# Optimization experiments

Measured on AMD Instinct MI355X. Metric: run time of the kernel, lower is better.

## Reference

```python
import jax, jax.numpy as jnp
import numpy as np
import math

D = 1024
B, S = 8, 2048


def setup_inputs() -> dict:
    key = jax.random.key(0)
    ks = jax.random.split(key, 8)
    q = jax.random.normal(ks[0], (B, S, D), dtype=jnp.float32)
    k = jax.random.normal(ks[1], (B, S, D), dtype=jnp.float32)
    v1 = jax.random.normal(ks[2], (B, S, D), dtype=jnp.float32)
    mask = jax.random.normal(ks[3], (1, S, S), dtype=jnp.float32)
    # Linear params: torch Linear stores W as [out, in]; init ~ U(-1/sqrt(in), 1/sqrt(in))
    lim = 1.0 / math.sqrt(D)
    W1 = jax.random.uniform(ks[4], (D, D), jnp.float32, -lim, lim)
    b1 = jax.random.uniform(ks[5], (D,), jnp.float32, -lim, lim)
    W2 = jax.random.uniform(ks[6], (D, D), jnp.float32, -lim, lim)
    b2 = jax.random.uniform(ks[7], (D,), jnp.float32, -lim, lim)
    return {"q": q, "k": k, "v1": v1, "mask": mask,
            "W1": W1, "b1": b1, "W2": W2, "b2": b2}


def _proj(x, W1, b1, W2, b2):
    # linear2(linear1(x)); torch Linear: x @ W.T + b
    h = jnp.einsum('bsd,od->bso', x, W1) + b1
    return jnp.einsum('bsd,od->bso', h, W2) + b2


def reference(q, k, v1, mask, W1, b1, W2, b2):
    qp = _proj(q, W1, b1, W2, b2)          # [B,S,D]
    kp = _proj(k, W1, b1, W2, b2)          # [B,S,D]
    scale = 1.0 / math.sqrt(qp.shape[-1])
    qk = jnp.einsum('bqd,bkd->bqk', qp, kp) * scale  # [B,S,S]
    qk = qk + mask                          # broadcast [1,S,S]
    attn = jax.nn.softmax(qk, axis=-1)
    return jnp.einsum('bqk,bkd->bqd', attn, v1)  # [B,S,D]
```

## Files before the change

### kernel.cpp

```cpp
#include <hip/hip_runtime.h>
#include <hip/hip_bf16.h>

typedef __hip_bfloat16 bf16;
typedef short short8 __attribute__((ext_vector_type(8)));
typedef float f32x4 __attribute__((ext_vector_type(4)));

constexpr int Bn = 8, Sn = 2048, Dn = 1024;
constexpr int BM = 256, BN = 256, BK = 64;

__global__ void cast_f32_bf16_k(const float* __restrict__ x, bf16* __restrict__ y, int n) {
  int i = (blockIdx.x * blockDim.x + threadIdx.x) * 4;
  if (i >= n) return;
  float4 f = *reinterpret_cast<const float4*>(x + i);
  bf16 tmp[4] = {__float2bfloat16(f.x), __float2bfloat16(f.y),
                 __float2bfloat16(f.z), __float2bfloat16(f.w)};
  *reinterpret_cast<short4*>(y + i) = *reinterpret_cast<const short4*>(tmp);
}

__global__ void transpose_cast_v_k(const float* __restrict__ v, bf16* __restrict__ vt) {
  __shared__ float tile[32][33];
  const int s0 = blockIdx.x * 32, d0 = blockIdx.y * 32, b = blockIdx.z;
  const float* src = v + (size_t)b * Sn * Dn;
  bf16* dst = vt + (size_t)b * Dn * Sn;
  const int tx = threadIdx.x & 31, ty = threadIdx.x >> 5;
  #pragma unroll
  for (int i = 0; i < 4; ++i) {
    int s = ty + i * 8;
    tile[s][tx] = src[(size_t)(s0 + s) * Dn + d0 + tx];
  }
  __syncthreads();
  #pragma unroll
  for (int i = 0; i < 4; ++i) {
    int d = ty + i * 8;
    dst[(size_t)(d0 + d) * Sn + s0 + tx] = __float2bfloat16(tile[tx][d]);
  }
}

#define BARRIER() asm volatile("s_barrier" ::: "memory")
#define WAIT_VM8() asm volatile("s_waitcnt vmcnt(8)" ::: "memory")
#define WAIT_VM0() asm volatile("s_waitcnt vmcnt(0)" ::: "memory")

#define QUAD(ms, ns) do {                                                     \
    __builtin_amdgcn_s_setprio(1);                                            \
    _Pragma("unroll")                                                         \
    for (int kk = 0; kk < 2; ++kk) {                                          \
      _Pragma("unroll")                                                       \
      for (int mi4 = 0; mi4 < 4; ++mi4) {                                     \
        _Pragma("unroll")                                                     \
        for (int n2 = 0; n2 < 2; ++n2)                                        \
          asm volatile("v_mfma_f32_16x16x32_bf16 %0, %1, %2, %0"              \
                       : "+v"(acc[(ms)*4+mi4][(ns)*2+n2])                     \
                       : "v"(aF[mi4][kk]), "v"(bF[(ns)*2+n2][kk]));           \
      }                                                                       \
    }                                                                         \
    __builtin_amdgcn_s_setprio(0);                                            \
  } while (0)

#define RD_A(buf, ms) do {                                                    \
    _Pragma("unroll")                                                         \
    for (int mi4 = 0; mi4 < 4; ++mi4) {                                       \
      aF[mi4][0] = rdA(buf, ms, mi4, 0);                                      \
      aF[mi4][1] = rdA(buf, ms, mi4, 1);                                      \
    }                                                                         \
  } while (0)

#define RD_B(buf, ns) do {                                                    \
    bF[(ns)*2  ][0] = rdB(buf, ns, 0, 0);                                     \
    bF[(ns)*2  ][1] = rdB(buf, ns, 0, 1);                                     \
    bF[(ns)*2+1][0] = rdB(buf, ns, 1, 0);                                     \
    bF[(ns)*2+1][1] = rdB(buf, ns, 1, 1);                                     \
  } while (0)

#define TILE_BODY(cc, DS, Tn2, WAITCODE) do {                                 \
    RD_A(cc, 0); RD_B(cc, 0);                                                 \
    BARRIER(); QUAD(0, 0); BARRIER();                                         \
    RD_B(cc, 1);                                                              \
    BARRIER(); QUAD(0, 1); BARRIER();                                         \
    RD_A(cc, 1);                                                              \
    if (DS) stage(32768 + (cc)*16384, Bbase, 0, (Tn2));                       \
    BARRIER(); QUAD(1, 0); BARRIER();                                         \
    if (DS) { stage(32768 + (cc)*16384, Bbase, 1, (Tn2));                     \
              stage((cc)*16384,          Abase, 0, (Tn2));                    \
              stage((cc)*16384,          Abase, 1, (Tn2)); }                  \
    BARRIER(); QUAD(1, 1);                                                    \
    WAITCODE;                                                                 \
    BARRIER();                                                                \
  } while (0)

template<int EPI>
__global__ __launch_bounds__(512, 2)
void gemm256_k(const bf16* __restrict__ A, const bf16* __restrict__ BT,
               void* __restrict__ Cv, const float* __restrict__ aux,
               int N, int K, long long sAz, long long sBz, long long sCz,
               float scale, int gx, int gy)
{
  __shared__ __align__(128) bf16 sh[4 * 16384];

  const int nwg = (int)gridDim.x;
  const int flat = (int)blockIdx.x;
  const int swz = (flat & 7) * (nwg >> 3) + (flat >> 3);
  const int tn = swz % gx;
  const int rem = swz / gx;
  const int tm = rem % gy;
  const int z  = rem / gy;

  const int t = threadIdx.x, w = t >> 6, lane = t & 63;
  const int wm = w >> 2, wn = w & 3;
  const int fr = lane & 15, kg = lane >> 4;
  const int m0 = tm * BM, n0 = tn * BN;
  const bf16* Abase = A + (size_t)z * sAz + (size_t)m0 * K;
  const bf16* Bbase = BT + (size_t)z * sBz + (size_t)n0 * K;

  f32x4 acc[8][4];
  const f32x4 fz = {0.f, 0.f, 0.f, 0.f};
  #pragma unroll
  for (int i = 0; i < 8; ++i)
    #pragma unroll
    for (int j = 0; j < 4; ++j) acc[i][j] = fz;
  short8 aF[4][2], bF[4][2];

  auto stage = [&](int dstElemBase, const bf16* gbase, int half, int kt) {
    const bf16* g0 = gbase + (size_t)(half * 128) * K + (size_t)kt * BK;
    bf16* db = (bf16*)sh + dstElemBase + half * 8192;
    #pragma unroll
    for (int i = 0; i < 2; ++i) {
      const int s0 = i * 512 + w * 64;
      const int slot = s0 + lane;
      const int row = slot >> 3;
      const int cb = (slot & 7) ^ (row & 7);
      const bf16* src = g0 + (size_t)row * K + cb * 8;
      __builtin_amdgcn_global_load_lds((__attribute__((address_space(1))) void*)src,
          (__attribute__((address_space(3))) void*)(db + s0 * 8), 16, 0, 0);
    }
  };
  auto rdA = [&](int buf, int ms, int mi4, int kk) -> short8 {
    const int row = wm * 128 + ms * 64 + mi4 * 16 + fr;
    int loc = row * 128 + kk * 64 + kg * 16;
    loc ^= (row & 7) << 4;
    return *reinterpret_cast<const short8*>((const char*)sh + buf * 32768 + loc);
  };
  auto rdB = [&](int buf, int ns, int j, int kk) -> short8 {
    const int row = wn * 64 + ns * 32 + j * 16 + fr;
    int loc = row * 128 + kk * 64 + kg * 16;
    loc ^= (row & 7) << 4;
    return *reinterpret_cast<const short8*>((const char*)sh + 65536 + buf * 32768 + loc);
  };

  const int NT = K / BK;
  stage(32768, Bbase, 0, 0); stage(32768, Bbase, 1, 0);
  stage(0,     Abase, 0, 0); stage(0,     Abase, 1, 0);
  stage(49152, Bbase, 0, 1); stage(49152, Bbase, 1, 1);
  stage(16384, Abase, 0, 1); stage(16384, Abase, 1, 1);
  WAIT_VM8();
  BARRIER();

  int T = 0;
  for (; T < NT - 2; T += 2) {
    TILE_BODY(0, (T     < NT - 2), T + 2, WAIT_VM8());
    TILE_BODY(1, (T + 1 < NT - 2), T + 3, WAIT_VM8());
  }
  TILE_BODY(0, 0, 0, WAIT_VM0());
  TILE_BODY(1, 0, 0, (void)0);

  const int or0 = kg * 4;
  if constexpr (EPI == 0) {
    bf16* C = (bf16*)Cv + (size_t)z * sCz;
    #pragma unroll
    for (int mi = 0; mi < 8; ++mi)
      #pragma unroll
      for (int r = 0; r < 4; ++r) {
        const int row = m0 + wm * 128 + mi * 16 + or0 + r;
        #pragma unroll
        for (int ni = 0; ni < 4; ++ni) {
          const int col = n0 + wn * 64 + ni * 16 + fr;
          C[(size_t)row * N + col] = __float2bfloat16(acc[mi][ni][r] + aux[col]);
        }
      }
  } else if constexpr (EPI == 1) {
    bf16* C = (bf16*)Cv + (size_t)z * sCz;
    #pragma unroll
    for (int mi = 0; mi < 8; ++mi)
      #pragma unroll
      for (int r = 0; r < 4; ++r) {
        const int row = m0 + wm * 128 + mi * 16 + or0 + r;
        #pragma unroll
        for (int ni = 0; ni < 4; ++ni) {
          const int col = n0 + wn * 64 + ni * 16 + fr;
          float v = acc[mi][ni][r] * scale + aux[(size_t)row * N + col];
          C[(size_t)row * N + col] = __float2bfloat16(v);
        }
      }
  } else {
    float* C = (float*)Cv + (size_t)z * sCz;
    #pragma unroll
    for (int mi = 0; mi < 8; ++mi)
      #pragma unroll
      for (int r = 0; r < 4; ++r) {
        const int row = m0 + wm * 128 + mi * 16 + or0 + r;
        #pragma unroll
        for (int ni = 0; ni < 4; ++ni) {
          const int col = n0 + wn * 64 + ni * 16 + fr;
          C[(size_t)row * N + col] = acc[mi][ni][r];
        }
      }
  }
}

__global__ __launch_bounds__(256)
void softmax_rows_k(bf16* __restrict__ sc) {
  const size_t row = blockIdx.x;
  bf16* p = sc + row * (size_t)Sn;
  const int t = threadIdx.x;
  unsigned short raw[8];
  *reinterpret_cast<int4*>(raw) = *reinterpret_cast<const int4*>(p + t * 8);
  float x[8];
  float m = -1e30f;
  #pragma unroll
  for (int j = 0; j < 8; ++j) {
    x[j] = __uint_as_float(((unsigned)raw[j]) << 16);
    m = fmaxf(m, x[j]);
  }
  #pragma unroll
  for (int off = 32; off >= 1; off >>= 1) m = fmaxf(m, __shfl_xor(m, off));
  __shared__ float sred[4], ssum[4];
  const int w = t >> 6;
  if ((t & 63) == 0) sred[w] = m;
  __syncthreads();
  m = fmaxf(fmaxf(sred[0], sred[1]), fmaxf(sred[2], sred[3]));
  float e[8], s = 0.f;
  #pragma unroll
  for (int j = 0; j < 8; ++j) { e[j] = __expf(x[j] - m); s += e[j]; }
  #pragma unroll
  for (int off = 32; off >= 1; off >>= 1) s += __shfl_xor(s, off);
  if ((t & 63) == 0) ssum[w] = s;
  __syncthreads();
  s = (ssum[0] + ssum[1]) + (ssum[2] + ssum[3]);
  const float inv = 1.f / s;
  unsigned short o[8];
  #pragma unroll
  for (int j = 0; j < 8; ++j) {
    bf16 hv = __float2bfloat16(e[j] * inv);
    o[j] = *reinterpret_cast<unsigned short*>(&hv);
  }
  *reinterpret_cast<int4*>(p + t * 8) = *reinterpret_cast<const int4*>(o);
}

extern "C" void kernel_launch(void* const* d_in, const int* in_sizes, int n_in,
                              void* d_out, int out_size, void* d_ws, size_t ws_size,
                              hipStream_t stream) {
  const float* q    = (const float*)d_in[0];
  const float* k    = (const float*)d_in[1];
  const float* v1   = (const float*)d_in[2];
  const float* mask = (const float*)d_in[3];
  const float* W1   = (const float*)d_in[4];
  const float* b1   = (const float*)d_in[5];
  const float* W2   = (const float*)d_in[6];
  const float* b2   = (const float*)d_in[7];
  float* out = (float*)d_out;

  const size_t nQKD = (size_t)Bn * Sn * Dn;
  char* ws = (char*)d_ws;
  bf16* qkb = (bf16*)ws;
  bf16* qb  = qkb;
  bf16* kb  = qkb + nQKD;
  bf16* vtb = qkb + 2 * nQKD;
  bf16* hb  = vtb + nQKD;
  bf16* w1b = hb + 2 * nQKD;
  bf16* w2b = w1b + (size_t)Dn * Dn;
  bf16* scb = w2b + (size_t)Dn * Dn;

  dim3 blk(256);
  const int nQK = (int)nQKD;
  cast_f32_bf16_k<<<dim3(nQK / 4 / 256), blk, 0, stream>>>(q, qb, nQK);
  cast_f32_bf16_k<<<dim3(nQK / 4 / 256), blk, 0, stream>>>(k, kb, nQK);
  cast_f32_bf16_k<<<dim3(Dn * Dn / 4 / 256), blk, 0, stream>>>(W1, w1b, Dn * Dn);
  cast_f32_bf16_k<<<dim3(Dn * Dn / 4 / 256), blk, 0, stream>>>(W2, w2b, Dn * Dn);
  transpose_cast_v_k<<<dim3(Sn / 32, Dn / 32, Bn), blk, 0, stream>>>(v1, vtb);

  const int M2 = 2 * Bn * Sn;
  dim3 gblk(512);
  gemm256_k<0><<<dim3(4 * (M2 / BM)), gblk, 0, stream>>>(
      qkb, w1b, hb, b1, Dn, Dn, 0, 0, 0, 1.f, 4, M2 / BM);
  gemm256_k<0><<<dim3(4 * (M2 / BM)), gblk, 0, stream>>>(
      hb, w2b, qkb, b2, Dn, Dn, 0, 0, 0, 1.f, 4, M2 / BM);
  gemm256_k<1><<<dim3(8 * 8 * Bn), gblk, 0, stream>>>(
      qb, kb, scb, mask, Sn, Dn,
      (long long)Sn * Dn, (long long)Sn * Dn, (long long)Sn * Sn, 0.03125f, 8, 8);
  softmax_rows_k<<<dim3(Bn * Sn), blk, 0, stream>>>(scb);
  gemm256_k<2><<<dim3(4 * 8 * Bn), gblk, 0, stream>>>(
      scb, vtb, out, nullptr, Dn, Sn,
      (long long)Sn * Sn, (long long)Dn * Sn, (long long)Sn * Dn, 1.f, 4, 8);
}
```

Measured before the change: 398.3 us.

## Interleave global-to-LDS prefetch stages across each quadrant of the GEMM main loop

Restructures the 256x256 GEMM main loop so that the global_load_lds prefetches for A and B are spread one per MFMA quadrant instead of grouped, with staggered tiles (A for T+1, B for T+2) and a vmcnt(4) wait instead of vmcnt(8). It also replaces inline-asm MFMA with the compiler builtin and adds explicit lgkmcnt(0) waits before each quadrant. The aim is to smooth memory issue and let the compiler schedule MFMAs, at the cost of more barriers and waits that could stall the waves.

```diff
diff --git a/kernel.cpp b/kernel.cpp
--- a/kernel.cpp
+++ b/kernel.cpp
@@ -2,7 +2,7 @@
 #include <hip/hip_bf16.h>
 
 typedef __hip_bfloat16 bf16;
-typedef short short8 __attribute__((ext_vector_type(8)));
+typedef __bf16 bf16x8 __attribute__((ext_vector_type(8)));
 typedef float f32x4 __attribute__((ext_vector_type(4)));
 
 constexpr int Bn = 8, Sn = 2048, Dn = 1024;
@@ -36,23 +36,23 @@
   }
 }
 
-#define BARRIER() asm volatile("s_barrier" ::: "memory")
-#define WAIT_VM8() asm volatile("s_waitcnt vmcnt(8)" ::: "memory")
-#define WAIT_VM0() asm volatile("s_waitcnt vmcnt(0)" ::: "memory")
+#define SBAR()  asm volatile("s_barrier" ::: "memory")
+#define LGKM0() asm volatile("s_waitcnt lgkmcnt(0)" ::: "memory")
+#define VM4()   asm volatile("s_waitcnt vmcnt(4)" ::: "memory")
+#define VM0()   asm volatile("s_waitcnt vmcnt(0)" ::: "memory")
 
 #define QUAD(ms, ns) do {                                                     \
     __builtin_amdgcn_s_setprio(1);                                            \
     _Pragma("unroll")                                                         \
-    for (int kk = 0; kk < 2; ++kk) {                                          \
+    for (int kk = 0; kk < 2; ++kk)                                            \
       _Pragma("unroll")                                                       \
-      for (int mi4 = 0; mi4 < 4; ++mi4) {                                     \
+      for (int mi4 = 0; mi4 < 4; ++mi4)                                       \
         _Pragma("unroll")                                                     \
         for (int n2 = 0; n2 < 2; ++n2)                                        \
-          asm volatile("v_mfma_f32_16x16x32_bf16 %0, %1, %2, %0"              \
-                       : "+v"(acc[(ms)*4+mi4][(ns)*2+n2])                     \
-                       : "v"(aF[mi4][kk]), "v"(bF[(ns)*2+n2][kk]));           \
-      }                                                                       \
-    }                                                                         \
+          acc[(ms)*4+mi4][(ns)*2+n2] =                                        \
+            __builtin_amdgcn_mfma_f32_16x16x32_bf16(                          \
+              aF[mi4][kk], bF[(ns)*2+n2][kk],                                 \
+              acc[(ms)*4+mi4][(ns)*2+n2], 0, 0, 0);                           \
     __builtin_amdgcn_s_setprio(0);                                            \
   } while (0)
 
@@ -69,22 +69,6 @@
     bF[(ns)*2  ][1] = rdB(buf, ns, 0, 1);                                     \
     bF[(ns)*2+1][0] = rdB(buf, ns, 1, 0);                                     \
     bF[(ns)*2+1][1] = rdB(buf, ns, 1, 1);                                     \
-  } while (0)
-
-#define TILE_BODY(cc, DS, Tn2, WAITCODE) do {                                 \
-    RD_A(cc, 0); RD_B(cc, 0);                                                 \
-    BARRIER(); QUAD(0, 0); BARRIER();                                         \
-    RD_B(cc, 1);                                                              \
-    BARRIER(); QUAD(0, 1); BARRIER();                                         \
-    RD_A(cc, 1);                                                              \
-    if (DS) stage(32768 + (cc)*16384, Bbase, 0, (Tn2));                       \
-    BARRIER(); QUAD(1, 0); BARRIER();                                         \
-    if (DS) { stage(32768 + (cc)*16384, Bbase, 1, (Tn2));                     \
-              stage((cc)*16384,          Abase, 0, (Tn2));                    \
-              stage((cc)*16384,          Abase, 1, (Tn2)); }                  \
-    BARRIER(); QUAD(1, 1);                                                    \
-    WAITCODE;                                                                 \
-    BARRIER();                                                                \
   } while (0)
 
 template<int EPI>
@@ -117,7 +101,7 @@
   for (int i = 0; i < 8; ++i)
     #pragma unroll
     for (int j = 0; j < 4; ++j) acc[i][j] = fz;
-  short8 aF[4][2], bF[4][2];
+  bf16x8 aF[4][2], bF[4][2];
 
   auto stage = [&](int dstElemBase, const bf16* gbase, int half, int kt) {
     const bf16* g0 = gbase + (size_t)(half * 128) * K + (size_t)kt * BK;
@@ -133,34 +117,55 @@
           (__attribute__((address_space(3))) void*)(db + s0 * 8), 16, 0, 0);
     }
   };
-  auto rdA = [&](int buf, int ms, int mi4, int kk) -> short8 {
+  auto rdA = [&](int buf, int ms, int mi4, int kk) -> bf16x8 {
     const int row = wm * 128 + ms * 64 + mi4 * 16 + fr;
     int loc = row * 128 + kk * 64 + kg * 16;
     loc ^= (row & 7) << 4;
-    return *reinterpret_cast<const short8*>((const char*)sh + buf * 32768 + loc);
+    return *reinterpret_cast<const bf16x8*>((const char*)sh + buf * 32768 + loc);
   };
-  auto rdB = [&](int buf, int ns, int j, int kk) -> short8 {
+  auto rdB = [&](int buf, int ns, int j, int kk) -> bf16x8 {
     const int row = wn * 64 + ns * 32 + j * 16 + fr;
     int loc = row * 128 + kk * 64 + kg * 16;
     loc ^= (row & 7) << 4;
-    return *reinterpret_cast<const short8*>((const char*)sh + 65536 + buf * 32768 + loc);
+    return *reinterpret_cast<const bf16x8*>((const char*)sh + 65536 + buf * 32768 + loc);
   };
 
   const int NT = K / BK;
   stage(32768, Bbase, 0, 0); stage(32768, Bbase, 1, 0);
   stage(0,     Abase, 0, 0); stage(0,     Abase, 1, 0);
   stage(49152, Bbase, 0, 1); stage(49152, Bbase, 1, 1);
-  stage(16384, Abase, 0, 1); stage(16384, Abase, 1, 1);
-  WAIT_VM8();
-  BARRIER();
-
-  int T = 0;
-  for (; T < NT - 2; T += 2) {
-    TILE_BODY(0, (T     < NT - 2), T + 2, WAIT_VM8());
-    TILE_BODY(1, (T + 1 < NT - 2), T + 3, WAIT_VM8());
-  }
-  TILE_BODY(0, 0, 0, WAIT_VM0());
-  TILE_BODY(1, 0, 0, (void)0);
+  VM4();
+  SBAR();
+
+  for (int T = 0; T < NT; T += 2) {
+    const bool last = (T + 2 >= NT);
+    RD_A(0, 0); RD_B(0, 0);
+    stage(16384, Abase, 0, T + 1);
+    SBAR(); LGKM0(); QUAD(0, 0); SBAR();
+    RD_B(0, 1);
+    stage(16384, Abase, 1, T + 1);
+    SBAR(); LGKM0(); QUAD(0, 1); SBAR();
+    RD_A(0, 1);
+    if (!last) stage(32768, Bbase, 0, T + 2);
+    SBAR(); LGKM0(); QUAD(1, 0); SBAR();
+    if (!last) stage(32768, Bbase, 1, T + 2);
+    SBAR(); LGKM0(); QUAD(1, 1);
+    if (last) { VM0(); } else { VM4(); }
+    SBAR();
+    RD_A(1, 0); RD_B(1, 0);
+    if (!last) stage(0, Abase, 0, T + 2);
+    SBAR(); LGKM0(); QUAD(0, 0); SBAR();
+    RD_B(1, 1);
+    if (!last) stage(0, Abase, 1, T + 2);
+    SBAR(); LGKM0(); QUAD(0, 1); SBAR();
+    RD_A(1, 1);
+    if (!last) stage(49152, Bbase, 0, T + 3);
+    SBAR(); LGKM0(); QUAD(1, 0); SBAR();
+    if (!last) stage(49152, Bbase, 1, T + 3);
+    SBAR(); LGKM0(); QUAD(1, 1);
+    if (!last) { VM4(); }
+    SBAR();
+  }
 
   const int or0 = kg * 4;
   if constexpr (EPI == 0) {
```

Result: no change. 400.1 us (+0.5%).
